# Kernel tuning notes

Measured on AMD Instinct MI355X. Metric: run time of the kernel, lower is better.

## Reference

```python
import jax, jax.numpy as jnp
import numpy as np

LIMIT_A = -0.1
LIMIT_B = 1.1
MASK_INIT_MEAN = float(np.log(1 - 0.2) - np.log(0.2))  # droprate_init = 0.2

B, T, I, H = 64, 512, 1024, 1024


def _hard_concrete_gate(mask_logits):
    # deterministic (eval) gate: hardtanh(sigmoid(mask) * (limit_b - limit_a) + limit_a, 0, 1)
    return jnp.clip(jax.nn.sigmoid(mask_logits) * (LIMIT_B - LIMIT_A) + LIMIT_A, 0.0, 1.0)


def setup_inputs() -> dict:
    key = jax.random.key(0)
    ks = jax.random.split(key, 9)
    xavier = float(np.sqrt(6.0 / (H + I)))
    seq = jax.random.normal(ks[0], (B, T, I), dtype=jnp.float32)
    w_ih = jax.random.uniform(ks[1], (H, I), jnp.float32, -xavier, xavier)
    w_hh = jax.random.uniform(ks[2], (H, H), jnp.float32, -xavier, xavier)
    b_ih = jnp.zeros((H,), jnp.float32)
    b_hh = jnp.zeros((H,), jnp.float32)
    # mask logits ~ N(log((1-droprate)/droprate), 0.01)
    w_ih_mask = MASK_INIT_MEAN + 0.01 * jax.random.normal(ks[3], (H, I), jnp.float32)
    w_hh_mask = MASK_INIT_MEAN + 0.01 * jax.random.normal(ks[4], (H, H), jnp.float32)
    b_ih_mask = MASK_INIT_MEAN + 0.01 * jax.random.normal(ks[5], (H,), jnp.float32)
    b_hh_mask = MASK_INIT_MEAN + 0.01 * jax.random.normal(ks[6], (H,), jnp.float32)
    return {
        "seq": seq,
        "w_ih": w_ih, "w_ih_mask": w_ih_mask,
        "w_hh": w_hh, "w_hh_mask": w_hh_mask,
        "b_ih": b_ih, "b_ih_mask": b_ih_mask,
        "b_hh": b_hh, "b_hh_mask": b_hh_mask,
    }


def reference(seq, w_ih, w_ih_mask, w_hh, w_hh_mask, b_ih, b_ih_mask, b_hh, b_hh_mask):
    # gated (L0 hard-concrete, deterministic) weights
    W_ih = _hard_concrete_gate(w_ih_mask) * w_ih  # [H, I]
    W_hh = _hard_concrete_gate(w_hh_mask) * w_hh  # [H, H]
    B_ih = _hard_concrete_gate(b_ih_mask) * b_ih  # [H]
    B_hh = _hard_concrete_gate(b_hh_mask) * b_hh  # [H]

    # precompute input projection for all timesteps: [B, T, H]
    x_proj = jnp.einsum('bti,hi->bth', seq, W_ih) + B_ih + B_hh

    h0 = jnp.zeros((seq.shape[0], W_hh.shape[0]), seq.dtype)

    def step(h, xp_t):  # xp_t: [B, H]
        h_new = jnp.tanh(xp_t + h @ W_hh.T)
        return h_new, h_new

    h_last, hs = jax.lax.scan(step, h0, jnp.swapaxes(x_proj, 0, 1))  # hs: [T, B, H]
    output = jnp.swapaxes(hs, 0, 1)  # [B, T, H] (batch_first)
    return output, h_last[None]  # hidden: [num_layers*num_dirs, B, H]
```

## Files before the change

kernel.cpp:

```cpp
#include <hip/hip_runtime.h>
#include <cmath>


typedef _Float16 v8h __attribute__((ext_vector_type(8)));
typedef float    v4f __attribute__((ext_vector_type(4)));
typedef unsigned long long u64;

#define BB 64
#define TT 512
#define HH 1024
#define OUT_MAIN (BB * TT * HH)
#define OFF_WIH  0u
#define OFF_WHH  (2u << 20)
#define OFF_BIAS (4u << 20)
#define OFF_HBUF ((4u << 20) + 8192u)
#define OFF_SEQ  ((4u << 20) + 8192u + 262144u)

#define ALD(p)    __hip_atomic_load((p),        __ATOMIC_RELAXED, __HIP_MEMORY_SCOPE_AGENT)
#define AST(p, v) __hip_atomic_store((p), (v),  __ATOMIC_RELAXED, __HIP_MEMORY_SCOPE_AGENT)

__device__ __forceinline__ float hc_gate(float x) {
    float s = 1.0f / (1.0f + __expf(-x));
    float g = s * 1.2f - 0.1f;
    return fminf(1.0f, fmaxf(0.0f, g));
}

__device__ __forceinline__ float fast_tanh(float x) {
    float e = __expf(2.0f * x);
    return 1.0f - 2.0f * __builtin_amdgcn_rcpf(e + 1.0f);
}

__global__ void prep_kernel(const float* __restrict__ w_ih, const float* __restrict__ w_ih_mask,
                            const float* __restrict__ w_hh, const float* __restrict__ w_hh_mask,
                            const float* __restrict__ b_ih, const float* __restrict__ b_ih_mask,
                            const float* __restrict__ b_hh, const float* __restrict__ b_hh_mask,
                            _Float16* __restrict__ Wih, _Float16* __restrict__ Whh,
                            float* __restrict__ bias, _Float16* __restrict__ hbuf,
                            int* __restrict__ seqf) {
    const int idx = blockIdx.x * 256 + threadIdx.x;
    Wih[idx] = (_Float16)(hc_gate(w_ih_mask[idx]) * w_ih[idx]);
    Whh[idx] = (_Float16)(hc_gate(w_hh_mask[idx]) * w_hh[idx]);
    if (idx < HH)
        bias[idx] = hc_gate(b_ih_mask[idx]) * b_ih[idx] + hc_gate(b_hh_mask[idx]) * b_hh[idx];
    if (idx < 131072) hbuf[idx] = (_Float16)0.0f;
    if (idx < 256) seqf[idx] = 0;
}

__global__ __launch_bounds__(256, 2) void gemm_xproj(const float* __restrict__ seq,
                                                     const _Float16* __restrict__ Wih,
                                                     const float* __restrict__ bias,
                                                     float* __restrict__ out) {
    __shared__ _Float16 As[128][40];
    __shared__ _Float16 Bs[128][40];

    const int tid  = threadIdx.x;
    const int lane = tid & 63;
    const int w    = tid >> 6;
    const int bid  = blockIdx.x;
    const int m0 = (bid >> 3) * 128;
    const int n0 = (bid & 7) * 128;
    const int mw = (w >> 1) * 64, nw = (w & 1) * 64;

    const int sr = tid >> 1;
    const int sc = (tid & 1) * 16;

    const float*    aSrc = seq + (m0 + sr) * HH + sc;
    const _Float16* bSrc = Wih + (n0 + sr) * HH + sc;

    const v4f vzero = {0.f, 0.f, 0.f, 0.f};
    v4f acc[4][4];
#pragma unroll
    for (int i = 0; i < 4; i++)
#pragma unroll
        for (int j = 0; j < 4; j++) acc[i][j] = vzero;

    const int arow = mw + (lane & 15);
    const int brow = nw + (lane & 15);
    const int kq   = (lane >> 4) * 8;

    for (int k0 = 0; k0 < HH; k0 += 32) {
        float4 f0 = *(const float4*)(aSrc + 0);
        float4 f1 = *(const float4*)(aSrc + 4);
        float4 f2 = *(const float4*)(aSrc + 8);
        float4 f3 = *(const float4*)(aSrc + 12);
        v8h a0 = {(_Float16)f0.x, (_Float16)f0.y, (_Float16)f0.z, (_Float16)f0.w,
                  (_Float16)f1.x, (_Float16)f1.y, (_Float16)f1.z, (_Float16)f1.w};
        v8h a1 = {(_Float16)f2.x, (_Float16)f2.y, (_Float16)f2.z, (_Float16)f2.w,
                  (_Float16)f3.x, (_Float16)f3.y, (_Float16)f3.z, (_Float16)f3.w};
        v8h b0 = *(const v8h*)(bSrc + 0);
        v8h b1 = *(const v8h*)(bSrc + 8);
        *(v8h*)&As[sr][sc]     = a0;
        *(v8h*)&As[sr][sc + 8] = a1;
        *(v8h*)&Bs[sr][sc]     = b0;
        *(v8h*)&Bs[sr][sc + 8] = b1;
        __syncthreads();

        v8h af[4], bf[4];
#pragma unroll
        for (int mi = 0; mi < 4; mi++) af[mi] = *(const v8h*)&As[mi * 16 + arow][kq];
#pragma unroll
        for (int ni = 0; ni < 4; ni++) bf[ni] = *(const v8h*)&Bs[ni * 16 + brow][kq];
#pragma unroll
        for (int mi = 0; mi < 4; mi++)
#pragma unroll
            for (int ni = 0; ni < 4; ni++)
                acc[mi][ni] = __builtin_amdgcn_mfma_f32_16x16x32_f16(af[mi], bf[ni], acc[mi][ni], 0, 0, 0);
        __syncthreads();
        aSrc += 32;
        bSrc += 32;
    }

    const int colb = lane & 15;
    const int rowq = (lane >> 4) * 4;
#pragma unroll
    for (int ni = 0; ni < 4; ni++) {
        const int col = n0 + nw + ni * 16 + colb;
        const float bz = bias[col];
#pragma unroll
        for (int mi = 0; mi < 4; mi++) {
            const int row = m0 + mw + mi * 16 + rowq;
#pragma unroll
            for (int r = 0; r < 4; r++)
                out[(row + r) * HH + col] = acc[mi][ni][r] + bz;
        }
    }
}

__global__ __launch_bounds__(256, 1) void rnn_steps(const _Float16* __restrict__ Whh,
                                                    float* __restrict__ out,
                                                    _Float16* __restrict__ hbuf,
                                                    int* __restrict__ seqf) {
    __shared__ _Float16 tile[16 * 128];
    __shared__ __align__(16) u64 hlds[32 * 128];

    const int tid  = threadIdx.x;
    const int lane = tid & 63;
    const int w    = tid >> 6;
    const int bid  = blockIdx.x;
    const int g    = bid >> 3;
    const int jw   = bid & 7;

    const int l15 = lane & 15;
    const int kq  = (lane >> 4) * 8;
    const int bq  = (lane >> 4) * 4;

    const int col0 = jw * 128 + w * 32 + l15;

    v8h Wf[64];
    {
        const _Float16* w0 = Whh + col0 * 1024 + kq;
        const _Float16* w1 = Whh + (col0 + 16) * 1024 + kq;
#pragma unroll
        for (int c = 0; c < 32; c++) {
            Wf[c * 2 + 0] = *(const v8h*)(w0 + c * 32);
            Wf[c * 2 + 1] = *(const v8h*)(w1 + c * 32);
        }
    }

    {
        u64* q = &hlds[(jw * 4 + w) * 128 + lane * 2];
        q[0] = 0ull; q[1] = 0ull;
    }

    float xp[2][4];
#pragma unroll
    for (int r = 0; r < 4; r++) {
        const float* xs = out + ((g * 16 + bq + r) * TT + 0) * HH + col0;
        xp[0][r] = xs[0];
        xp[1][r] = xs[16];
    }

    const int pollIdx = (lane < 8 && lane != jw) ? (lane * 4 + w) : -1;

    for (int t = 0; t < TT; t++) {
        int* sqp = seqf + ((t & 1) * 4 + g) * 32;

        for (;;) {
            int ok = 1;
            if (pollIdx >= 0) ok = (ALD(sqp + pollIdx) >= t) ? 1 : 0;
            if (__all(ok)) break;
            __builtin_amdgcn_s_sleep(1);
        }
        asm volatile("" ::: "memory");

        {
            const u64* hbp = (const u64*)(hbuf + ((t & 1) * 4 + g) * 16384);
            u64 dv[16];
#pragma unroll
            for (int i = 0; i < 8; i++) {
                if (i != jw) {
                    const u64* p = hbp + (i * 4 + w) * 128 + lane * 2;
                    dv[2 * i]     = ALD(p);
                    dv[2 * i + 1] = ALD(p + 1);
                }
            }
#pragma unroll
            for (int i = 0; i < 8; i++) {
                if (i != jw) {
                    u64* q = &hlds[(i * 4 + w) * 128 + lane * 2];
                    q[0] = dv[2 * i];
                    q[1] = dv[2 * i + 1];
                }
            }
        }
        __syncthreads();

        v4f aA0 = {0.f, 0.f, 0.f, 0.f}, aA1 = aA0, aB0 = aA0, aB1 = aA0;
#pragma unroll
        for (int cc = 0; cc < 8; cc++) {
            const u64* q = &hlds[cc * 512 + lane * 2];
            v8h h0 = *(const v8h*)(q);
            v8h h1 = *(const v8h*)(q + 128);
            v8h h2 = *(const v8h*)(q + 256);
            v8h h3 = *(const v8h*)(q + 384);
            aA0 = __builtin_amdgcn_mfma_f32_16x16x32_f16(h0, Wf[(cc * 4 + 0) * 2 + 0], aA0, 0, 0, 0);
            aA1 = __builtin_amdgcn_mfma_f32_16x16x32_f16(h0, Wf[(cc * 4 + 0) * 2 + 1], aA1, 0, 0, 0);
            aB0 = __builtin_amdgcn_mfma_f32_16x16x32_f16(h1, Wf[(cc * 4 + 1) * 2 + 0], aB0, 0, 0, 0);
            aB1 = __builtin_amdgcn_mfma_f32_16x16x32_f16(h1, Wf[(cc * 4 + 1) * 2 + 1], aB1, 0, 0, 0);
            aA0 = __builtin_amdgcn_mfma_f32_16x16x32_f16(h2, Wf[(cc * 4 + 2) * 2 + 0], aA0, 0, 0, 0);
            aA1 = __builtin_amdgcn_mfma_f32_16x16x32_f16(h2, Wf[(cc * 4 + 2) * 2 + 1], aA1, 0, 0, 0);
            aB0 = __builtin_amdgcn_mfma_f32_16x16x32_f16(h3, Wf[(cc * 4 + 3) * 2 + 0], aB0, 0, 0, 0);
            aB1 = __builtin_amdgcn_mfma_f32_16x16x32_f16(h3, Wf[(cc * 4 + 3) * 2 + 1], aB1, 0, 0, 0);
        }
        const v4f av0 = aA0 + aB0;
        const v4f av1 = aA1 + aB1;

        float hv[2][4];
#pragma unroll
        for (int r = 0; r < 4; r++) {
            hv[0][r] = fast_tanh(xp[0][r] + av0[r]);
            hv[1][r] = fast_tanh(xp[1][r] + av1[r]);
            const int row = bq + r;
            const int sw  = (row & 7) << 4;
            char* base = (char*)tile + row * 256;
            *(_Float16*)(base + (((w * 32 + l15) * 2) ^ sw))      = (_Float16)hv[0][r];
            *(_Float16*)(base + (((w * 32 + 16 + l15) * 2) ^ sw)) = (_Float16)hv[1][r];
        }
        __syncthreads();

        {
            const int row = lane & 15;
            const int cb  = (w * 32 + (lane >> 4) * 8) * 2;
            union { v8h v; u64 u[2]; } uu;
            uu.v = *(const v8h*)((const char*)tile + row * 256 + (cb ^ ((row & 7) << 4)));
            u64* dst = (u64*)(hbuf + (((t + 1) & 1) * 4 + g) * 16384) + (jw * 4 + w) * 128 + lane * 2;
            AST(dst,     uu.u[0]);
            AST(dst + 1, uu.u[1]);
            u64* q = &hlds[(jw * 4 + w) * 128 + lane * 2];
            q[0] = uu.u[0];
            q[1] = uu.u[1];
        }
        asm volatile("s_waitcnt vmcnt(0)" ::: "memory");
        if (lane == 0)
            AST(seqf + (((t + 1) & 1) * 4 + g) * 32 + jw * 4 + w, t + 1);

#pragma unroll
        for (int r = 0; r < 4; r++) {
            const int bg = g * 16 + bq + r;
            float* o = out + (bg * TT + t) * HH + col0;
            o[0]  = hv[0][r];
            o[16] = hv[1][r];
            if (t == TT - 1) {
                float* o2 = out + OUT_MAIN + bg * HH + col0;
                o2[0]  = hv[0][r];
                o2[16] = hv[1][r];
            }
        }
        if (t + 1 < TT) {
#pragma unroll
            for (int r = 0; r < 4; r++) {
                const float* xs = out + ((g * 16 + bq + r) * TT + (t + 1)) * HH + col0;
                xp[0][r] = xs[0];
                xp[1][r] = xs[16];
            }
        }
    }
}

extern "C" void kernel_launch(void* const* d_in, const int* in_sizes, int n_in,
                              void* d_out, int out_size, void* d_ws, size_t ws_size,
                              hipStream_t stream) {
    const float* seq       = (const float*)d_in[0];
    const float* w_ih      = (const float*)d_in[1];
    const float* w_ih_mask = (const float*)d_in[2];
    const float* w_hh      = (const float*)d_in[3];
    const float* w_hh_mask = (const float*)d_in[4];
    const float* b_ih      = (const float*)d_in[5];
    const float* b_ih_mask = (const float*)d_in[6];
    const float* b_hh      = (const float*)d_in[7];
    const float* b_hh_mask = (const float*)d_in[8];

    float* out = (float*)d_out;
    char*  ws  = (char*)d_ws;
    _Float16* Wih  = (_Float16*)(ws + OFF_WIH);
    _Float16* Whh  = (_Float16*)(ws + OFF_WHH);
    float*    bias = (float*)(ws + OFF_BIAS);
    _Float16* hbuf = (_Float16*)(ws + OFF_HBUF);
    int*      seqf = (int*)(ws + OFF_SEQ);

    prep_kernel<<<dim3(4096), dim3(256), 0, stream>>>(w_ih, w_ih_mask, w_hh, w_hh_mask,
                                                      b_ih, b_ih_mask, b_hh, b_hh_mask,
                                                      Wih, Whh, bias, hbuf, seqf);
    gemm_xproj<<<dim3(2048), dim3(256), 0, stream>>>(seq, Wih, bias, out);
    rnn_steps<<<dim3(32), dim3(256), 0, stream>>>(Whh, out, hbuf, seqf);
}
```

Before: 2.320 ms.

## Tag hidden-state exchange words with step number to drop separate flag handshake

Replaces the separate per-wave sequence-flag array and its store-fence-flag protocol with a tagged buffer. Each 32-bit half of the fp16 hidden state is packed alongside the step number in a 64-bit atomic word. Consumers poll the data words directly until every tag reaches the current step, which removes the vmcnt(0) wait and the extra flag round trip on the recurrent critical path. The cost is twice the exchange traffic and more polling loads per spin iteration.

```diff
diff --git a/kernel.cpp b/kernel.cpp
--- a/kernel.cpp
+++ b/kernel.cpp
@@ -5,6 +5,7 @@
 typedef _Float16 v8h __attribute__((ext_vector_type(8)));
 typedef float    v4f __attribute__((ext_vector_type(4)));
 typedef unsigned long long u64;
+typedef unsigned int u32;
 
 #define BB 64
 #define TT 512
@@ -14,7 +15,6 @@
 #define OFF_WHH  (2u << 20)
 #define OFF_BIAS (4u << 20)
 #define OFF_HBUF ((4u << 20) + 8192u)
-#define OFF_SEQ  ((4u << 20) + 8192u + 262144u)
 
 #define ALD(p)    __hip_atomic_load((p),        __ATOMIC_RELAXED, __HIP_MEMORY_SCOPE_AGENT)
 #define AST(p, v) __hip_atomic_store((p), (v),  __ATOMIC_RELAXED, __HIP_MEMORY_SCOPE_AGENT)
@@ -35,15 +35,13 @@
                             const float* __restrict__ b_ih, const float* __restrict__ b_ih_mask,
                             const float* __restrict__ b_hh, const float* __restrict__ b_hh_mask,
                             _Float16* __restrict__ Wih, _Float16* __restrict__ Whh,
-                            float* __restrict__ bias, _Float16* __restrict__ hbuf,
-                            int* __restrict__ seqf) {
+                            float* __restrict__ bias, u64* __restrict__ hbt) {
     const int idx = blockIdx.x * 256 + threadIdx.x;
     Wih[idx] = (_Float16)(hc_gate(w_ih_mask[idx]) * w_ih[idx]);
     Whh[idx] = (_Float16)(hc_gate(w_hh_mask[idx]) * w_hh[idx]);
     if (idx < HH)
         bias[idx] = hc_gate(b_ih_mask[idx]) * b_ih[idx] + hc_gate(b_hh_mask[idx]) * b_hh[idx];
-    if (idx < 131072) hbuf[idx] = (_Float16)0.0f;
-    if (idx < 256) seqf[idx] = 0;
+    if (idx < 65536) hbt[idx] = 0ull;
 }
 
 __global__ __launch_bounds__(256, 2) void gemm_xproj(const float* __restrict__ seq,
@@ -128,8 +126,7 @@
 
 __global__ __launch_bounds__(256, 1) void rnn_steps(const _Float16* __restrict__ Whh,
                                                     float* __restrict__ out,
-                                                    _Float16* __restrict__ hbuf,
-                                                    int* __restrict__ seqf) {
+                                                    u64* __restrict__ hbt) {
     __shared__ _Float16 tile[16 * 128];
     __shared__ __align__(16) u64 hlds[32 * 128];
 
@@ -170,37 +167,52 @@
         xp[1][r] = xs[16];
     }
 
-    const int pollIdx = (lane < 8 && lane != jw) ? (lane * 4 + w) : -1;
-
     for (int t = 0; t < TT; t++) {
-        int* sqp = seqf + ((t & 1) * 4 + g) * 32;
-
+        const u64* tb = hbt + (u64)(((t & 1) * 4 + g) * 32) * 256;
+        u64 d[8][4];
+#pragma unroll
+        for (int i = 0; i < 8; i++) {
+            if (i != jw) {
+                const u64* p = tb + (i * 4 + w) * 256 + lane;
+                d[i][0] = ALD(p);       d[i][1] = ALD(p + 64);
+                d[i][2] = ALD(p + 128); d[i][3] = ALD(p + 192);
+            }
+        }
+        const u32 tt = (u32)t;
         for (;;) {
             int ok = 1;
-            if (pollIdx >= 0) ok = (ALD(sqp + pollIdx) >= t) ? 1 : 0;
+#pragma unroll
+            for (int i = 0; i < 8; i++) {
+                if (i != jw) {
+                    u32 m0 = (u32)(d[i][0] >> 32), m1 = (u32)(d[i][1] >> 32);
+                    u32 m2 = (u32)(d[i][2] >> 32), m3 = (u32)(d[i][3] >> 32);
+                    u32 a = m0 < m1 ? m0 : m1;
+                    u32 b = m2 < m3 ? m2 : m3;
+                    u32 mn = a < b ? a : b;
+                    ok &= (mn >= tt) ? 1 : 0;
+                }
+            }
             if (__all(ok)) break;
             __builtin_amdgcn_s_sleep(1);
-        }
-        asm volatile("" ::: "memory");
-
-        {
-            const u64* hbp = (const u64*)(hbuf + ((t & 1) * 4 + g) * 16384);
-            u64 dv[16];
 #pragma unroll
             for (int i = 0; i < 8; i++) {
                 if (i != jw) {
-                    const u64* p = hbp + (i * 4 + w) * 128 + lane * 2;
-                    dv[2 * i]     = ALD(p);
-                    dv[2 * i + 1] = ALD(p + 1);
+                    const u64* p = tb + (i * 4 + w) * 256 + lane;
+                    d[i][0] = ALD(p);       d[i][1] = ALD(p + 64);
+                    d[i][2] = ALD(p + 128); d[i][3] = ALD(p + 192);
                 }
             }
-#pragma unroll
-            for (int i = 0; i < 8; i++) {
-                if (i != jw) {
-                    u64* q = &hlds[(i * 4 + w) * 128 + lane * 2];
-                    q[0] = dv[2 * i];
-                    q[1] = dv[2 * i + 1];
-                }
+        }
+        asm volatile("" ::: "memory");
+
+#pragma unroll
+        for (int i = 0; i < 8; i++) {
+            if (i != jw) {
+                u64 lo = (d[i][0] & 0xffffffffull) | (d[i][1] << 32);
+                u64 hi = (d[i][2] & 0xffffffffull) | (d[i][3] << 32);
+                u64* q = &hlds[(i * 4 + w) * 128 + lane * 2];
+                q[0] = lo;
+                q[1] = hi;
             }
         }
         __syncthreads();
@@ -243,16 +255,16 @@
             const int cb  = (w * 32 + (lane >> 4) * 8) * 2;
             union { v8h v; u64 u[2]; } uu;
             uu.v = *(const v8h*)((const char*)tile + row * 256 + (cb ^ ((row & 7) << 4)));
-            u64* dst = (u64*)(hbuf + (((t + 1) & 1) * 4 + g) * 16384) + (jw * 4 + w) * 128 + lane * 2;
-            AST(dst,     uu.u[0]);
-            AST(dst + 1, uu.u[1]);
+            u64* dstb = hbt + (u64)((((t + 1) & 1) * 4 + g) * 32 + jw * 4 + w) * 256 + lane;
+            const u64 tg = ((u64)(u32)(t + 1)) << 32;
+            AST(dstb,       tg | (u64)(u32)uu.u[0]);
+            AST(dstb + 64,  tg | (uu.u[0] >> 32));
+            AST(dstb + 128, tg | (u64)(u32)uu.u[1]);
+            AST(dstb + 192, tg | (uu.u[1] >> 32));
             u64* q = &hlds[(jw * 4 + w) * 128 + lane * 2];
             q[0] = uu.u[0];
             q[1] = uu.u[1];
         }
-        asm volatile("s_waitcnt vmcnt(0)" ::: "memory");
-        if (lane == 0)
-            AST(seqf + (((t + 1) & 1) * 4 + g) * 32 + jw * 4 + w, t + 1);
 
 #pragma unroll
         for (int r = 0; r < 4; r++) {
@@ -295,12 +307,11 @@
     _Float16* Wih  = (_Float16*)(ws + OFF_WIH);
     _Float16* Whh  = (_Float16*)(ws + OFF_WHH);
     float*    bias = (float*)(ws + OFF_BIAS);
-    _Float16* hbuf = (_Float16*)(ws + OFF_HBUF);
-    int*      seqf = (int*)(ws + OFF_SEQ);
+    u64*      hbt  = (u64*)(ws + OFF_HBUF);
 
     prep_kernel<<<dim3(4096), dim3(256), 0, stream>>>(w_ih, w_ih_mask, w_hh, w_hh_mask,
                                                       b_ih, b_ih_mask, b_hh, b_hh_mask,
-                                                      Wih, Whh, bias, hbuf, seqf);
+                                                      Wih, Whh, bias, hbt);
     gemm_xproj<<<dim3(2048), dim3(256), 0, stream>>>(seq, Wih, bias, out);
-    rnn_steps<<<dim3(32), dim3(256), 0, stream>>>(Whh, out, hbuf, seqf);
-}
+    rnn_steps<<<dim3(32), dim3(256), 0, stream>>>(Whh, out, hbt);
+}
```

Measured after the change: 2.895 ms. +24.8%, slower.

## Fuse input-projection GEMM and recurrence into one kernel with per-chunk readiness counters

Applied to the files above, without the earlier changes.

Merges the x-projection GEMM and the sequential RNN kernel into a single launch. Blocks 0-31 run the recurrence while the remaining blocks compute the GEMM in time-chunks of 128 steps, each chunk signalling completion through atomic counters that the recurrent blocks poll before reading the next chunk. This lets the recurrence overlap with the GEMM instead of waiting for all of it. The h-exchange also moves to per-wave LDS tiles so the global publish and flag store happen before the block barrier. The risks are that GEMM blocks compete with the 32 recurrent blocks for CUs and bandwidth, and that the design relies on all 32 recurrent blocks being resident so the spin-waits cannot deadlock.

```diff
diff --git a/kernel.cpp b/kernel.cpp
--- a/kernel.cpp
+++ b/kernel.cpp
@@ -5,6 +5,7 @@
 typedef _Float16 v8h __attribute__((ext_vector_type(8)));
 typedef float    v4f __attribute__((ext_vector_type(4)));
 typedef unsigned long long u64;
+typedef unsigned int u32;
 
 #define BB 64
 #define TT 512
@@ -14,7 +15,8 @@
 #define OFF_WHH  (2u << 20)
 #define OFF_BIAS (4u << 20)
 #define OFF_HBUF ((4u << 20) + 8192u)
-#define OFF_SEQ  ((4u << 20) + 8192u + 262144u)
+#define OFF_SEQF ((4u << 20) + 8192u + 262144u)
+#define OFF_CNT  ((4u << 20) + 8192u + 262144u + 1024u)
 
 #define ALD(p)    __hip_atomic_load((p),        __ATOMIC_RELAXED, __HIP_MEMORY_SCOPE_AGENT)
 #define AST(p, v) __hip_atomic_store((p), (v),  __ATOMIC_RELAXED, __HIP_MEMORY_SCOPE_AGENT)
@@ -36,7 +38,7 @@
                             const float* __restrict__ b_hh, const float* __restrict__ b_hh_mask,
                             _Float16* __restrict__ Wih, _Float16* __restrict__ Whh,
                             float* __restrict__ bias, _Float16* __restrict__ hbuf,
-                            int* __restrict__ seqf) {
+                            int* __restrict__ seqf, int* __restrict__ cnt) {
     const int idx = blockIdx.x * 256 + threadIdx.x;
     Wih[idx] = (_Float16)(hc_gate(w_ih_mask[idx]) * w_ih[idx]);
     Whh[idx] = (_Float16)(hc_gate(w_hh_mask[idx]) * w_hh[idx]);
@@ -44,101 +46,112 @@
         bias[idx] = hc_gate(b_ih_mask[idx]) * b_ih[idx] + hc_gate(b_hh_mask[idx]) * b_hh[idx];
     if (idx < 131072) hbuf[idx] = (_Float16)0.0f;
     if (idx < 256) seqf[idx] = 0;
-}
-
-__global__ __launch_bounds__(256, 2) void gemm_xproj(const float* __restrict__ seq,
-                                                     const _Float16* __restrict__ Wih,
-                                                     const float* __restrict__ bias,
-                                                     float* __restrict__ out) {
-    __shared__ _Float16 As[128][40];
-    __shared__ _Float16 Bs[128][40];
+    if (idx < 128) cnt[idx] = 0;
+}
+
+__global__ __launch_bounds__(256, 1) void fused_kernel(
+        const float* __restrict__ seq, const _Float16* __restrict__ Wih,
+        const _Float16* __restrict__ Whh, const float* __restrict__ bias,
+        float* __restrict__ out, _Float16* __restrict__ hbuf,
+        int* __restrict__ seqf, int* __restrict__ cnt) {
+    __shared__ __align__(16) char smem[38912];
 
     const int tid  = threadIdx.x;
     const int lane = tid & 63;
     const int w    = tid >> 6;
-    const int bid  = blockIdx.x;
-    const int m0 = (bid >> 3) * 128;
-    const int n0 = (bid & 7) * 128;
-    const int mw = (w >> 1) * 64, nw = (w & 1) * 64;
-
-    const int sr = tid >> 1;
-    const int sc = (tid & 1) * 16;
-
-    const float*    aSrc = seq + (m0 + sr) * HH + sc;
-    const _Float16* bSrc = Wih + (n0 + sr) * HH + sc;
-
-    const v4f vzero = {0.f, 0.f, 0.f, 0.f};
-    v4f acc[4][4];
-#pragma unroll
-    for (int i = 0; i < 4; i++)
-#pragma unroll
-        for (int j = 0; j < 4; j++) acc[i][j] = vzero;
-
-    const int arow = mw + (lane & 15);
-    const int brow = nw + (lane & 15);
-    const int kq   = (lane >> 4) * 8;
-
-    for (int k0 = 0; k0 < HH; k0 += 32) {
-        float4 f0 = *(const float4*)(aSrc + 0);
-        float4 f1 = *(const float4*)(aSrc + 4);
-        float4 f2 = *(const float4*)(aSrc + 8);
-        float4 f3 = *(const float4*)(aSrc + 12);
-        v8h a0 = {(_Float16)f0.x, (_Float16)f0.y, (_Float16)f0.z, (_Float16)f0.w,
-                  (_Float16)f1.x, (_Float16)f1.y, (_Float16)f1.z, (_Float16)f1.w};
-        v8h a1 = {(_Float16)f2.x, (_Float16)f2.y, (_Float16)f2.z, (_Float16)f2.w,
-                  (_Float16)f3.x, (_Float16)f3.y, (_Float16)f3.z, (_Float16)f3.w};
-        v8h b0 = *(const v8h*)(bSrc + 0);
-        v8h b1 = *(const v8h*)(bSrc + 8);
-        *(v8h*)&As[sr][sc]     = a0;
-        *(v8h*)&As[sr][sc + 8] = a1;
-        *(v8h*)&Bs[sr][sc]     = b0;
-        *(v8h*)&Bs[sr][sc + 8] = b1;
+
+    if (blockIdx.x >= 32) {
+        _Float16 (*As)[40] = (_Float16 (*)[40])smem;
+        _Float16 (*Bs)[40] = (_Float16 (*)[40])(smem + 10240);
+
+        const int gbid   = blockIdx.x - 32;
+        const int trange = gbid >> 9;
+        const int rem    = gbid & 511;
+        const int bb     = rem >> 3;
+        const int njw    = rem & 7;
+        const int m0 = bb * 512 + trange * 128;
+        const int n0 = njw * 128;
+        const int mw = (w >> 1) * 64, nw = (w & 1) * 64;
+
+        const int sr = tid >> 1;
+        const int sc = (tid & 1) * 16;
+
+        const float*    aSrc = seq + (m0 + sr) * HH + sc;
+        const _Float16* bSrc = Wih + (n0 + sr) * HH + sc;
+
+        const v4f vzero = {0.f, 0.f, 0.f, 0.f};
+        v4f acc[4][4];
+#pragma unroll
+        for (int i = 0; i < 4; i++)
+#pragma unroll
+            for (int j = 0; j < 4; j++) acc[i][j] = vzero;
+
+        const int arow = mw + (lane & 15);
+        const int brow = nw + (lane & 15);
+        const int kq   = (lane >> 4) * 8;
+
+        for (int k0 = 0; k0 < HH; k0 += 32) {
+            float4 f0 = *(const float4*)(aSrc + 0);
+            float4 f1 = *(const float4*)(aSrc + 4);
+            float4 f2 = *(const float4*)(aSrc + 8);
+            float4 f3 = *(const float4*)(aSrc + 12);
+            v8h a0 = {(_Float16)f0.x, (_Float16)f0.y, (_Float16)f0.z, (_Float16)f0.w,
+                      (_Float16)f1.x, (_Float16)f1.y, (_Float16)f1.z, (_Float16)f1.w};
+            v8h a1 = {(_Float16)f2.x, (_Float16)f2.y, (_Float16)f2.z, (_Float16)f2.w,
+                      (_Float16)f3.x, (_Float16)f3.y, (_Float16)f3.z, (_Float16)f3.w};
+            v8h b0 = *(const v8h*)(bSrc + 0);
+            v8h b1 = *(const v8h*)(bSrc + 8);
+            *(v8h*)&As[sr][sc]     = a0;
+            *(v8h*)&As[sr][sc + 8] = a1;
+            *(v8h*)&Bs[sr][sc]     = b0;
+            *(v8h*)&Bs[sr][sc + 8] = b1;
+            __syncthreads();
+
+            v8h af[4], bf[4];
+#pragma unroll
+            for (int mi = 0; mi < 4; mi++) af[mi] = *(const v8h*)&As[mi * 16 + arow][kq];
+#pragma unroll
+            for (int ni = 0; ni < 4; ni++) bf[ni] = *(const v8h*)&Bs[ni * 16 + brow][kq];
+#pragma unroll
+            for (int mi = 0; mi < 4; mi++)
+#pragma unroll
+                for (int ni = 0; ni < 4; ni++)
+                    acc[mi][ni] = __builtin_amdgcn_mfma_f32_16x16x32_f16(af[mi], bf[ni], acc[mi][ni], 0, 0, 0);
+            __syncthreads();
+            aSrc += 32;
+            bSrc += 32;
+        }
+
+        const int colb = lane & 15;
+        const int rowq = (lane >> 4) * 4;
+#pragma unroll
+        for (int ni = 0; ni < 4; ni++) {
+            const int col = n0 + nw + ni * 16 + colb;
+            const float bz = bias[col];
+#pragma unroll
+            for (int mi = 0; mi < 4; mi++) {
+                const int row = m0 + mw + mi * 16 + rowq;
+#pragma unroll
+                for (int r = 0; r < 4; r++) {
+                    union { float f; u32 u; } cv;
+                    cv.f = acc[mi][ni][r] + bz;
+                    AST((u32*)&out[(row + r) * HH + col], cv.u);
+                }
+            }
+        }
         __syncthreads();
-
-        v8h af[4], bf[4];
-#pragma unroll
-        for (int mi = 0; mi < 4; mi++) af[mi] = *(const v8h*)&As[mi * 16 + arow][kq];
-#pragma unroll
-        for (int ni = 0; ni < 4; ni++) bf[ni] = *(const v8h*)&Bs[ni * 16 + brow][kq];
-#pragma unroll
-        for (int mi = 0; mi < 4; mi++)
-#pragma unroll
-            for (int ni = 0; ni < 4; ni++)
-                acc[mi][ni] = __builtin_amdgcn_mfma_f32_16x16x32_f16(af[mi], bf[ni], acc[mi][ni], 0, 0, 0);
-        __syncthreads();
-        aSrc += 32;
-        bSrc += 32;
-    }
-
-    const int colb = lane & 15;
-    const int rowq = (lane >> 4) * 4;
-#pragma unroll
-    for (int ni = 0; ni < 4; ni++) {
-        const int col = n0 + nw + ni * 16 + colb;
-        const float bz = bias[col];
-#pragma unroll
-        for (int mi = 0; mi < 4; mi++) {
-            const int row = m0 + mw + mi * 16 + rowq;
-#pragma unroll
-            for (int r = 0; r < 4; r++)
-                out[(row + r) * HH + col] = acc[mi][ni][r] + bz;
-        }
-    }
-}
-
-__global__ __launch_bounds__(256, 1) void rnn_steps(const _Float16* __restrict__ Whh,
-                                                    float* __restrict__ out,
-                                                    _Float16* __restrict__ hbuf,
-                                                    int* __restrict__ seqf) {
-    __shared__ _Float16 tile[16 * 128];
-    __shared__ __align__(16) u64 hlds[32 * 128];
-
-    const int tid  = threadIdx.x;
-    const int lane = tid & 63;
-    const int w    = tid >> 6;
-    const int bid  = blockIdx.x;
-    const int g    = bid >> 3;
-    const int jw   = bid & 7;
+        if (tid == 0)
+            __hip_atomic_fetch_add(&cnt[trange * 32 + (bb >> 4) * 8 + njw], 1,
+                                   __ATOMIC_RELAXED, __HIP_MEMORY_SCOPE_AGENT);
+        return;
+    }
+
+    u64*      hlds  = (u64*)smem;
+    _Float16* tbase = (_Float16*)(smem + 32768);
+
+    const int bid = blockIdx.x;
+    const int g   = bid >> 3;
+    const int jw  = bid & 7;
 
     const int l15 = lane & 15;
     const int kq  = (lane >> 4) * 8;
@@ -162,19 +175,25 @@
         q[0] = 0ull; q[1] = 0ull;
     }
 
+    {
+        const int* c0 = &cnt[0 * 32 + g * 8 + jw];
+        while (ALD(c0) < 16) __builtin_amdgcn_s_sleep(8);
+        asm volatile("" ::: "memory");
+    }
     float xp[2][4];
 #pragma unroll
     for (int r = 0; r < 4; r++) {
-        const float* xs = out + ((g * 16 + bq + r) * TT + 0) * HH + col0;
-        xp[0][r] = xs[0];
-        xp[1][r] = xs[16];
+        const u32* xs = (const u32*)(out + ((g * 16 + bq + r) * TT + 0) * HH + col0);
+        union { u32 u; float f; } v0, v1;
+        v0.u = ALD(xs); v1.u = ALD(xs + 16);
+        xp[0][r] = v0.f; xp[1][r] = v1.f;
     }
 
     const int pollIdx = (lane < 8 && lane != jw) ? (lane * 4 + w) : -1;
+    _Float16* tw = tbase + w * 640;
 
     for (int t = 0; t < TT; t++) {
         int* sqp = seqf + ((t & 1) * 4 + g) * 32;
-
         for (;;) {
             int ok = 1;
             if (pollIdx >= 0) ok = (ALD(sqp + pollIdx) >= t) ? 1 : 0;
@@ -231,28 +250,27 @@
             hv[0][r] = fast_tanh(xp[0][r] + av0[r]);
             hv[1][r] = fast_tanh(xp[1][r] + av1[r]);
             const int row = bq + r;
-            const int sw  = (row & 7) << 4;
-            char* base = (char*)tile + row * 256;
-            *(_Float16*)(base + (((w * 32 + l15) * 2) ^ sw))      = (_Float16)hv[0][r];
-            *(_Float16*)(base + (((w * 32 + 16 + l15) * 2) ^ sw)) = (_Float16)hv[1][r];
+            tw[row * 40 + l15]      = (_Float16)hv[0][r];
+            tw[row * 40 + 16 + l15] = (_Float16)hv[1][r];
+        }
+        union { v8h v; u64 u[2]; } U;
+        U.v = *(const v8h*)(tw + (lane & 15) * 40 + (lane >> 4) * 8);
+
+        if (t + 1 < TT) {
+            u64* dst = (u64*)(hbuf + (((t + 1) & 1) * 4 + g) * 16384) + (jw * 4 + w) * 128 + lane * 2;
+            AST(dst,     U.u[0]);
+            AST(dst + 1, U.u[1]);
+            asm volatile("s_waitcnt vmcnt(0)" ::: "memory");
+            if (lane == 0)
+                AST(seqf + (((t + 1) & 1) * 4 + g) * 32 + jw * 4 + w, t + 1);
         }
         __syncthreads();
 
         {
-            const int row = lane & 15;
-            const int cb  = (w * 32 + (lane >> 4) * 8) * 2;
-            union { v8h v; u64 u[2]; } uu;
-            uu.v = *(const v8h*)((const char*)tile + row * 256 + (cb ^ ((row & 7) << 4)));
-            u64* dst = (u64*)(hbuf + (((t + 1) & 1) * 4 + g) * 16384) + (jw * 4 + w) * 128 + lane * 2;
-            AST(dst,     uu.u[0]);
-            AST(dst + 1, uu.u[1]);
             u64* q = &hlds[(jw * 4 + w) * 128 + lane * 2];
-            q[0] = uu.u[0];
-            q[1] = uu.u[1];
-        }
-        asm volatile("s_waitcnt vmcnt(0)" ::: "memory");
-        if (lane == 0)
-            AST(seqf + (((t + 1) & 1) * 4 + g) * 32 + jw * 4 + w, t + 1);
+            q[0] = U.u[0];
+            q[1] = U.u[1];
+        }
 
 #pragma unroll
         for (int r = 0; r < 4; r++) {
@@ -267,11 +285,17 @@
             }
         }
         if (t + 1 < TT) {
+            if (((t + 1) & 127) == 0) {
+                const int* cc = &cnt[((t + 1) >> 7) * 32 + g * 8 + jw];
+                while (ALD(cc) < 16) __builtin_amdgcn_s_sleep(8);
+                asm volatile("" ::: "memory");
+            }
 #pragma unroll
             for (int r = 0; r < 4; r++) {
-                const float* xs = out + ((g * 16 + bq + r) * TT + (t + 1)) * HH + col0;
-                xp[0][r] = xs[0];
-                xp[1][r] = xs[16];
+                const u32* xs = (const u32*)(out + ((g * 16 + bq + r) * TT + (t + 1)) * HH + col0);
+                union { u32 u; float f; } v0, v1;
+                v0.u = ALD(xs); v1.u = ALD(xs + 16);
+                xp[0][r] = v0.f; xp[1][r] = v1.f;
             }
         }
     }
@@ -296,11 +320,12 @@
     _Float16* Whh  = (_Float16*)(ws + OFF_WHH);
     float*    bias = (float*)(ws + OFF_BIAS);
     _Float16* hbuf = (_Float16*)(ws + OFF_HBUF);
-    int*      seqf = (int*)(ws + OFF_SEQ);
+    int*      seqf = (int*)(ws + OFF_SEQF);
+    int*      cnt  = (int*)(ws + OFF_CNT);
 
     prep_kernel<<<dim3(4096), dim3(256), 0, stream>>>(w_ih, w_ih_mask, w_hh, w_hh_mask,
                                                       b_ih, b_ih_mask, b_hh, b_hh_mask,
-                                                      Wih, Whh, bias, hbuf, seqf);
-    gemm_xproj<<<dim3(2048), dim3(256), 0, stream>>>(seq, Wih, bias, out);
-    rnn_steps<<<dim3(32), dim3(256), 0, stream>>>(Whh, out, hbuf, seqf);
-}
+                                                      Wih, Whh, bias, hbuf, seqf, cnt);
+    fused_kernel<<<dim3(2080), dim3(256), 0, stream>>>(seq, Wih, Whh, bias, out,
+                                                       hbuf, seqf, cnt);
+}
```

New measurement: 2.175 ms (median of 2 runs). -6.3%, faster.
